# Kernel optimization log

Hardware: AMD Instinct MI355X
Metric: run time of the kernel (lower is better)

Reference implementation:

```python
import jax, jax.numpy as jnp
import numpy as np


def setup_inputs() -> dict:
    key = jax.random.key(0)
    ks = jax.random.split(key, 20)
    B, N, C = 8, 16384, 3

    def w(k, shape, scale=0.1):
        return jax.random.normal(k, shape, dtype=jnp.float32) * scale

    inp = {
        "points": jax.random.normal(ks[0], (B, N, C), dtype=jnp.float32),
        # first_layer: Conv1d(3,64,k=1)+BN+ReLU  (BN folded to scale s, shift t)
        "w0": w(ks[1], (64, 3)), "b0": w(ks[2], (64,)),
        "s0": 1.0 + w(ks[3], (64,), 0.05), "t0": w(ks[4], (64,), 0.05),
        # mlp1[3:]: Conv1d(64,64,k=1)+BN+ReLU
        "w1": w(ks[5], (64, 64)), "b1": w(ks[6], (64,)),
        "s1": 1.0 + w(ks[7], (64,), 0.05), "t1": w(ks[8], (64,), 0.05),
        # mlp2: Conv1d(64,128)+BN+ReLU, Conv1d(128,1024)+BN+ReLU
        "w2": w(ks[9], (128, 64)), "b2": w(ks[10], (128,)),
        "s2": 1.0 + w(ks[11], (128,), 0.05), "t2": w(ks[12], (128,), 0.05),
        "w3": w(ks[13], (1024, 128)), "b3": w(ks[14], (1024,)),
        "s3": 1.0 + w(ks[15], (1024,), 0.05), "t3": w(ks[16], (1024,), 0.05),
        "M": 512,
        "R": 32,
    }
    return inp


def _block(h, w, b, s, t):
    # pointwise Conv1d (k=1) + eval-mode BatchNorm (folded affine) + ReLU
    y = jnp.einsum('bmri,oi->bmro', h, w) + b
    return jax.nn.relu(y * s + t)


def reference(points, w0, b0, s0, t0, w1, b1, s1, t1,
              w2, b2, s2, t2, w3, b3, s3, t3, M, R):
    B, N, C = points.shape
    xyz = points[..., :3]
    barange = jnp.arange(B)

    # --- sampling: iteratively pick point farthest from the LAST centroid
    # (faithful to the original, which uses only centroids[i], not min-dist FPS)
    def step(last, _):
        d = jnp.sqrt(jnp.sum((xyz - last[:, None, :3]) ** 2, axis=-1))  # [B,N]
        ind = jnp.argmax(d, axis=-1)                                    # [B]
        new = points[barange, ind]                                      # [B,C]
        return new, new

    first = points[:, 0]  # deterministic stand-in for the random initial index
    _, rest = jax.lax.scan(step, first, None, length=M - 1)
    centroids = jnp.concatenate(
        [first[:, None], jnp.swapaxes(rest, 0, 1)], axis=1)  # [B,M,C]

    # --- grouping: R nearest points to each centroid
    d = jnp.sqrt(jnp.sum(
        (xyz[:, None] - centroids[:, :, None, :3]) ** 2, axis=-1))  # [B,M,N]
    _, idx = jax.lax.top_k(-d, R)                                    # [B,M,R]
    groups = points[barange[:, None, None], idx]                     # [B,M,R,C]

    # --- pointnet: shared pointwise MLP + max over group, vectorized over M
    h = _block(groups, w0, b0, s0, t0)   # [B,M,R,64]
    h = _block(h, w1, b1, s1, t1)        # [B,M,R,64]
    h = _block(h, w2, b2, s2, t2)        # [B,M,R,128]
    h = _block(h, w3, b3, s3, t3)        # [B,M,R,1024]
    g = jnp.max(h, axis=2)               # [B,M,1024]
    return g[..., None]                  # [B,M,1024,1]
```

## Files before the change

### kernel.cpp

```cpp
#include <hip/hip_runtime.h>

#define NPT 16384
#define MC  512
#define BATCH 8
#define CAP 512
#define LCAP 128

typedef __attribute__((ext_vector_type(8))) __bf16 bf16x8;
typedef __attribute__((ext_vector_type(4))) float f32x4;
typedef __attribute__((ext_vector_type(16))) float f32x16;
typedef __attribute__((ext_vector_type(2))) float f32x2;

static __device__ __forceinline__ unsigned short f2bf(float f) {
    unsigned int u = __float_as_uint(f);
    unsigned int r = (u + 0x7FFFu + ((u >> 16) & 1u)) >> 16;
    return (unsigned short)r;
}

static __device__ __forceinline__ float dist2(float x, float y, float z,
                                              float cx, float cy, float cz) {
    float dx = x - cx, dy = y - cy, dz = z - cz;
    return __fadd_rn(__fadd_rn(__fmul_rn(dx, dx), __fmul_rn(dy, dy)), __fmul_rn(dz, dz));
}

static __device__ __forceinline__ void dist2_pair(f32x2 x, f32x2 y, f32x2 z,
                                                  float cx, float cy, float cz,
                                                  float& d0, float& d1) {
    float dx0 = x[0] - cx, dx1 = x[1] - cx;
    float dy0 = y[0] - cy, dy1 = y[1] - cy;
    float dz0 = z[0] - cz, dz1 = z[1] - cz;
    float a0 = __fmul_rn(dx0, dx0), a1 = __fmul_rn(dx1, dx1);
    float b0 = __fmul_rn(dy0, dy0), b1 = __fmul_rn(dy1, dy1);
    float c0 = __fmul_rn(dz0, dz0), c1 = __fmul_rn(dz1, dz1);
    d0 = __fadd_rn(__fadd_rn(a0, b0), c0);
    d1 = __fadd_rn(__fadd_rn(a1, b1), c1);
}

__global__ void prep_all(const float* __restrict__ points,
                         const float* __restrict__ w1, const float* __restrict__ b1,
                         const float* __restrict__ s1, const float* __restrict__ t1,
                         const float* __restrict__ w2, const float* __restrict__ b2,
                         const float* __restrict__ s2, const float* __restrict__ t2,
                         const float* __restrict__ w3, const float* __restrict__ b3,
                         const float* __restrict__ s3, const float* __restrict__ t3,
                         unsigned short* __restrict__ Wp1, unsigned short* __restrict__ Wp2,
                         unsigned short* __restrict__ Wp3,
                         float* __restrict__ bias1, float* __restrict__ bias2,
                         float* __restrict__ bias3, float* __restrict__ soa,
                         int* __restrict__ gcnt) {
    int i = blockIdx.x * blockDim.x + threadIdx.x;
    if (i < 64 * 64) {
        int o = i >> 6;
        Wp1[i] = f2bf(w1[i] * s1[o]);
    } else if (i < 64 * 64 + 128 * 64) {
        int j = i - 4096; int o = j >> 6;
        Wp2[j] = f2bf(w2[j] * s2[o]);
    } else if (i < 64 * 64 + 128 * 64 + 1024 * 128) {
        int j = i - 12288; int o = j >> 7; int col = j & 127;
        int scol = (((col >> 3) ^ (o & 7)) << 3) | (col & 7);
        Wp3[j] = f2bf(w3[(o << 7) | scol] * s3[o]);
    }
    if (i < 64)   bias1[i] = b1[i] * s1[i] + t1[i];
    if (i < 128)  bias2[i] = b2[i] * s2[i] + t2[i];
    if (i < 1024) bias3[i] = b3[i] * s3[i] + t3[i];
    if (i < BATCH * MC) gcnt[i] = 0;
    if (i < BATCH * NPT) {
        int b = i >> 14, j = i & (NPT - 1);
        const float* p = points + ((size_t)b * NPT + j) * 3;
        float* s = soa + (size_t)b * 3 * NPT;
        s[j] = p[0];
        s[NPT + j] = p[1];
        s[2 * NPT + j] = p[2];
    }
}

__global__ __launch_bounds__(1024) void fps_kernel(const float* __restrict__ pts,
                                                   float* __restrict__ cent) {
    int b = blockIdx.x;
    const float* P = pts + (size_t)b * NPT * 3;
    float* C = cent + (size_t)b * MC * 3;
    __shared__ int hist[MC];
    __shared__ float curx, cury, curz;
    __shared__ float rd[16];
    __shared__ int ri[16];
    __shared__ int s_found, s_j;

    int tid = threadIdx.x;
    int i0 = tid * 16;
    float px[16], py[16], pz[16];
#pragma unroll
    for (int j = 0; j < 16; j++) {
        px[j] = P[(i0 + j) * 3 + 0];
        py[j] = P[(i0 + j) * 3 + 1];
        pz[j] = P[(i0 + j) * 3 + 2];
    }
    if (tid == 0) {
        hist[0] = 0;
        curx = P[0]; cury = P[1]; curz = P[2];
        C[0] = P[0]; C[1] = P[1]; C[2] = P[2];
        s_found = 0; s_j = 0;
    }
    __syncthreads();

    int t;
    for (t = 1; t < MC; t++) {
        float cx = curx, cy = cury, cz = curz;
        float bd = -1.0f; int bi = 0;
#pragma unroll
        for (int j = 0; j < 16; j++) {
            float dx = px[j] - cx, dy = py[j] - cy, dz = pz[j] - cz;
            float d2 = __fadd_rn(__fadd_rn(__fmul_rn(dx, dx), __fmul_rn(dy, dy)), __fmul_rn(dz, dz));
            float d = __fsqrt_rn(d2);
            if (d > bd) { bd = d; bi = i0 + j; }
        }
#pragma unroll
        for (int off = 32; off; off >>= 1) {
            float od = __shfl_xor(bd, off);
            int   oi = __shfl_xor(bi, off);
            if (od > bd || (od == bd && oi < bi)) { bd = od; bi = oi; }
        }
        int wid = tid >> 6;
        if ((tid & 63) == 0) { rd[wid] = bd; ri[wid] = bi; }
        __syncthreads();
        if (tid == 0) {
            float fb = rd[0]; int fi = ri[0];
            for (int wv = 1; wv < 16; wv++)
                if (rd[wv] > fb || (rd[wv] == fb && ri[wv] < fi)) { fb = rd[wv]; fi = ri[wv]; }
            int found = -1;
            for (int j = 0; j < t; j++) if (hist[j] == fi) { found = j; break; }
            hist[t] = fi;
            s_j = found;
            curx = P[fi * 3]; cury = P[fi * 3 + 1]; curz = P[fi * 3 + 2];
            C[t * 3] = curx; C[t * 3 + 1] = cury; C[t * 3 + 2] = curz;
            s_found = (found >= 0);
        }
        __syncthreads();
        if (s_found) break;
    }
    if (s_found && t < MC - 1) {
        int j = s_j, p = t - s_j;
        for (int k = t + 1 + tid; k < MC; k += 1024) {
            int src = j + (k - j) % p;
            int ind = hist[src];
            C[k * 3] = P[ind * 3]; C[k * 3 + 1] = P[ind * 3 + 1]; C[k * 3 + 2] = P[ind * 3 + 2];
        }
    }
}

__global__ __launch_bounds__(256) void bound_gather_kernel(
    const float* __restrict__ soa, const float* __restrict__ cent,
    int* __restrict__ gcnt, unsigned long long* __restrict__ gcand) {
    int tid = threadIdx.x, wv = tid >> 6, lane = tid & 63;
    int blk = blockIdx.x;
    int grp = blk >> 2;
    int chunk = blk & 3;
    int b = grp >> 6;
    int gbase = grp * 8;
    const float* Px = soa + (size_t)b * 3 * NPT + chunk * 4096;
    const float* Py = Px + NPT;
    const float* Pz = Py + NPT;

    __shared__ float smin[8][256];
    __shared__ unsigned int sU[8];
    __shared__ int lcnt[8];
    __shared__ unsigned long long lcand[8][LCAP];
    __shared__ int gslot[8];

    if (tid < 8) lcnt[tid] = 0;

    float cx[8], cy[8], cz[8];
#pragma unroll
    for (int c = 0; c < 8; c++) {
        cx[c] = __uint_as_float(__builtin_amdgcn_readfirstlane(__float_as_uint(cent[(size_t)(gbase + c) * 3 + 0])));
        cy[c] = __uint_as_float(__builtin_amdgcn_readfirstlane(__float_as_uint(cent[(size_t)(gbase + c) * 3 + 1])));
        cz[c] = __uint_as_float(__builtin_amdgcn_readfirstlane(__float_as_uint(cent[(size_t)(gbase + c) * 3 + 2])));
    }

    float lmin[8];
#pragma unroll
    for (int c = 0; c < 8; c++) lmin[c] = 3.4e38f;
#pragma unroll 2
    for (int k = 0; k < 8; k++) {
        int i = tid * 2 + k * 512;
        f32x2 x = *(const f32x2*)&Px[i];
        f32x2 y = *(const f32x2*)&Py[i];
        f32x2 z = *(const f32x2*)&Pz[i];
#pragma unroll
        for (int c = 0; c < 8; c++) {
            float d0, d1;
            dist2_pair(x, y, z, cx[c], cy[c], cz[c], d0, d1);
            lmin[c] = fminf(lmin[c], fminf(d0, d1));
        }
    }
#pragma unroll
    for (int c = 0; c < 8; c++) smin[c][tid] = lmin[c];
    __syncthreads();

    for (int cc = 0; cc < 2; ++cc) {
        int c = wv * 2 + cc;
        float4 q = *(const float4*)&smin[c][lane << 2];
        float m = fminf(fminf(q.x, q.y), fminf(q.z, q.w));
        unsigned int mb = __float_as_uint(m);
        unsigned int T = 0;
#pragma unroll
        for (int bit = 30; bit >= 0; --bit) {
            unsigned int cnd = T | (1u << bit);
            int cnt = __popcll(__ballot(mb < cnd));
            if (cnt <= 31) T = cnd;
        }
        float s = __fsqrt_rn(__uint_as_float(T));
        unsigned int u = T;
        for (int it = 0; it < 8 && __fsqrt_rn(__uint_as_float(u + 1u)) <= s; ++it) u++;
        if (lane == 0) sU[c] = u;
    }
    __syncthreads();
    unsigned int U[8];
#pragma unroll
    for (int c = 0; c < 8; c++) U[c] = sU[c];

#pragma unroll 2
    for (int k = 0; k < 8; k++) {
        int i = tid * 2 + k * 512;
        f32x2 x = *(const f32x2*)&Px[i];
        f32x2 y = *(const f32x2*)&Py[i];
        f32x2 z = *(const f32x2*)&Pz[i];
        unsigned int gi = (unsigned int)(chunk * 4096 + i);
#pragma unroll
        for (int c = 0; c < 8; c++) {
            float d0, d1;
            dist2_pair(x, y, z, cx[c], cy[c], cz[c], d0, d1);
            if (__float_as_uint(d0) <= U[c]) {
                int p = atomicAdd(&lcnt[c], 1);
                if (p < LCAP) {
                    unsigned int sb = __float_as_uint(__fsqrt_rn(d0));
                    lcand[c][p] = ((unsigned long long)sb << 32) | gi;
                }
            }
            if (__float_as_uint(d1) <= U[c]) {
                int p = atomicAdd(&lcnt[c], 1);
                if (p < LCAP) {
                    unsigned int sb = __float_as_uint(__fsqrt_rn(d1));
                    lcand[c][p] = ((unsigned long long)sb << 32) | (gi + 1u);
                }
            }
        }
    }
    __syncthreads();

    if (tid < 8) {
        int c = tid, n = lcnt[c];
        int add = (n > LCAP) ? 1000000 : n;
        gslot[c] = atomicAdd(&gcnt[gbase + c], add);
    }
    __syncthreads();
    for (int cc = 0; cc < 2; ++cc) {
        int c = wv * 2 + cc;
        int n = lcnt[c] < LCAP ? lcnt[c] : LCAP;
        int base = gslot[c];
        for (int q = lane; q < n; q += 64) {
            int pos = base + q;
            if (pos < CAP) gcand[(size_t)(gbase + c) * CAP + pos] = lcand[c][q];
        }
    }
}

__global__ __launch_bounds__(256) void select_l0_kernel(
    const float* __restrict__ soa, const float* __restrict__ cent,
    const int* __restrict__ gcnt, const unsigned long long* __restrict__ gcand,
    const float* __restrict__ w0, const float* __restrict__ b0,
    const float* __restrict__ s0, const float* __restrict__ t0,
    unsigned short* __restrict__ h0) {
    int tid = threadIdx.x, wv = tid >> 6, lane = tid & 63;
    int g = blockIdx.x * 4 + wv;
    int b = g >> 9;
    const float* Px = soa + (size_t)b * 3 * NPT;
    const float* Py = Px + NPT;
    const float* Pz = Py + NPT;

    __shared__ unsigned long long scand[4][CAP];
    __shared__ float sxyz[4][32][3];

    int n = gcnt[g];
    int nc = n < CAP ? n : CAP;
    for (int q = lane; q < nc; q += 64) scand[wv][q] = gcand[(size_t)g * CAP + q];

    unsigned long long sel = 0, last = 0;
    if (n <= CAP) {
        for (int s = 0; s < 32; s++) {
            unsigned long long best = ~0ull;
            for (int q = lane; q < nc; q += 64) {
                unsigned long long kk = scand[wv][q];
                if ((s == 0 || kk > last) && kk < best) best = kk;
            }
#pragma unroll
            for (int off = 32; off; off >>= 1) {
                unsigned long long o = __shfl_xor(best, off);
                best = o < best ? o : best;
            }
            last = best;
            if (lane == s) sel = best;
        }
    } else {
        for (int s = 0; s < 32; s++) {
            unsigned long long best = ~0ull;
            float ccx = cent[(size_t)g * 3], ccy = cent[(size_t)g * 3 + 1], ccz = cent[(size_t)g * 3 + 2];
            for (int i = lane; i < NPT; i += 64) {
                float d2 = dist2(Px[i], Py[i], Pz[i], ccx, ccy, ccz);
                unsigned int db = __float_as_uint(__fsqrt_rn(d2));
                unsigned long long kk = ((unsigned long long)db << 32) | (unsigned int)i;
                if ((s == 0 || kk > last) && kk < best) best = kk;
            }
#pragma unroll
            for (int off = 32; off; off >>= 1) {
                unsigned long long o = __shfl_xor(best, off);
                best = o < best ? o : best;
            }
            last = best;
            if (lane == s) sel = best;
        }
    }
    if (lane < 32) {
        unsigned int idx = (unsigned int)sel;
        if (idx >= NPT) idx = 0;
        sxyz[wv][lane][0] = Px[idx];
        sxyz[wv][lane][1] = Py[idx];
        sxyz[wv][lane][2] = Pz[idx];
    }

    int o = lane;
    float sw = s0[o];
    float fw0 = w0[o * 3] * sw, fw1 = w0[o * 3 + 1] * sw, fw2 = w0[o * 3 + 2] * sw;
    float fb = b0[o] * sw + t0[o];
    size_t base = ((size_t)g * 32) * 64 + o;
#pragma unroll 8
    for (int r = 0; r < 32; r++) {
        float x = sxyz[wv][r][0], y = sxyz[wv][r][1], z = sxyz[wv][r][2];
        float acc = fmaf(z, fw2, fmaf(y, fw1, fmaf(x, fw0, fb)));
        h0[base + (size_t)r * 64] = f2bf(fmaxf(acc, 0.0f));
    }
}

template <int N>
__global__ __launch_bounds__(256) void gemm_relu_kernel(
    const unsigned short* __restrict__ A, const unsigned short* __restrict__ W,
    const float* __restrict__ bias, unsigned short* __restrict__ Out) {
    __shared__ unsigned short sW[N * 64];
    int tid = threadIdx.x, w = tid >> 6, lane = tid & 63, lr = lane & 15, lq = lane >> 4;
    const int SWEEPS = (N * 64 * 2) / 4096;
#pragma unroll
    for (int sweep = 0; sweep < SWEEPS; ++sweep) {
        int r = sweep * 32 + (tid >> 3), s = tid & 7;
        int ss = s ^ (r & 7);
        *(uint4*)&sW[r * 64 + s * 8] = *(const uint4*)&W[r * 64 + ss * 8];
    }
    __syncthreads();

    int row0 = blockIdx.x * 256 + w * 64;
    const int NT = N / 16;
    f32x4 acc[4][NT];
#pragma unroll
    for (int m = 0; m < 4; m++)
#pragma unroll
        for (int n = 0; n < NT; n++) acc[m][n] = (f32x4){0.f, 0.f, 0.f, 0.f};

    bf16x8 a[4][2];
#pragma unroll
    for (int m = 0; m < 4; m++)
#pragma unroll
        for (int ks = 0; ks < 2; ks++)
            a[m][ks] = *(const bf16x8*)&A[(size_t)(row0 + m * 16 + lr) * 64 + ks * 32 + lq * 8];

#pragma unroll
    for (int ks = 0; ks < 2; ks++)
#pragma unroll
        for (int n = 0; n < NT; n++) {
            bf16x8 wf = *(const bf16x8*)&sW[(n * 16 + lr) * 64 + (((ks * 4 + lq) ^ (lr & 7)) * 8)];
#pragma unroll
            for (int m = 0; m < 4; m++)
                acc[m][n] = __builtin_amdgcn_mfma_f32_16x16x32_bf16(a[m][ks], wf, acc[m][n], 0, 0, 0);
        }

#pragma unroll
    for (int n = 0; n < NT; n++) {
        int col = n * 16 + lr;
        float bb = bias[col];
#pragma unroll
        for (int m = 0; m < 4; m++)
#pragma unroll
            for (int i = 0; i < 4; i++) {
                int rr = row0 + m * 16 + lq * 4 + i;
                Out[(size_t)rr * N + col] = f2bf(fmaxf(acc[m][n][i] + bb, 0.f));
            }
    }
}

__global__ __launch_bounds__(256) void gemm3_max_kernel(
    const unsigned short* __restrict__ A, const unsigned short* __restrict__ W,
    const float* __restrict__ bias, float* __restrict__ Out) {
    __shared__ unsigned short sW[128 * 128];
    int tid = threadIdx.x, w = tid >> 6, lane = tid & 63;
    int l32 = lane & 31, hi = lane >> 5;
    int wr = w >> 1, wc = w & 1;
    int row0 = blockIdx.x * 128 + wr * 64;
    int g0 = row0 >> 5;

    bf16x8 a[2][8];
#pragma unroll
    for (int m = 0; m < 2; m++)
#pragma unroll
        for (int ks = 0; ks < 8; ks++)
            a[m][ks] = *(const bf16x8*)&A[(size_t)(row0 + m * 32 + l32) * 128 + ks * 16 + hi * 8];

    for (int cb = 0; cb < 8; ++cb) {
#pragma unroll
        for (int j = 0; j < 8; ++j) {
            const unsigned short* g = W + (size_t)cb * 16384 + w * 4096 + j * 512 + lane * 8;
            __builtin_amdgcn_global_load_lds(
                (const __attribute__((address_space(1))) void*)g,
                (__attribute__((address_space(3))) void*)&sW[w * 4096 + j * 512],
                16, 0, 0);
        }
        __syncthreads();

        f32x16 acc[2][2];
#pragma unroll
        for (int m = 0; m < 2; m++)
#pragma unroll
            for (int n = 0; n < 2; n++)
#pragma unroll
                for (int r = 0; r < 16; r++) acc[m][n][r] = 0.f;

#pragma unroll
        for (int ks = 0; ks < 8; ks++)
#pragma unroll
            for (int n = 0; n < 2; n++) {
                int rw = wc * 64 + n * 32 + l32;
                int slot = (ks * 2 + hi) ^ (rw & 7);
                bf16x8 wf = *(const bf16x8*)&sW[rw * 128 + slot * 8];
#pragma unroll
                for (int m = 0; m < 2; m++)
                    acc[m][n] = __builtin_amdgcn_mfma_f32_32x32x16_bf16(a[m][ks], wf, acc[m][n], 0, 0, 0);
            }

#pragma unroll
        for (int n = 0; n < 2; n++) {
            int col = cb * 128 + wc * 64 + n * 32 + l32;
            float bb = bias[col];
#pragma unroll
            for (int m = 0; m < 2; m++) {
                float t0_ = fmaxf(acc[m][n][0], acc[m][n][1]);
                float t1_ = fmaxf(acc[m][n][2], acc[m][n][3]);
                float t2_ = fmaxf(acc[m][n][4], acc[m][n][5]);
                float t3_ = fmaxf(acc[m][n][6], acc[m][n][7]);
                float t4_ = fmaxf(acc[m][n][8], acc[m][n][9]);
                float t5_ = fmaxf(acc[m][n][10], acc[m][n][11]);
                float t6_ = fmaxf(acc[m][n][12], acc[m][n][13]);
                float t7_ = fmaxf(acc[m][n][14], acc[m][n][15]);
                float u0 = fmaxf(t0_, t1_), u1 = fmaxf(t2_, t3_);
                float u2 = fmaxf(t4_, t5_), u3 = fmaxf(t6_, t7_);
                float v = fmaxf(fmaxf(u0, u1), fmaxf(u2, u3));
                v = fmaxf(v, __shfl_xor(v, 32));
                v = fmaxf(v + bb, 0.f);
                if (hi == 0) Out[(size_t)(g0 + m) * 1024 + col] = v;
            }
        }
        __syncthreads();
    }
}

extern "C" void kernel_launch(void* const* d_in, const int* in_sizes, int n_in,
                              void* d_out, int out_size, void* d_ws, size_t ws_size,
                              hipStream_t stream) {
    const float* points = (const float*)d_in[0];
    const float* w0 = (const float*)d_in[1];
    const float* b0 = (const float*)d_in[2];
    const float* s0 = (const float*)d_in[3];
    const float* t0 = (const float*)d_in[4];
    const float* w1 = (const float*)d_in[5];
    const float* b1 = (const float*)d_in[6];
    const float* s1 = (const float*)d_in[7];
    const float* t1 = (const float*)d_in[8];
    const float* w2 = (const float*)d_in[9];
    const float* b2 = (const float*)d_in[10];
    const float* s2 = (const float*)d_in[11];
    const float* t2 = (const float*)d_in[12];
    const float* w3 = (const float*)d_in[13];
    const float* b3 = (const float*)d_in[14];
    const float* s3 = (const float*)d_in[15];
    const float* t3 = (const float*)d_in[16];

    char* ws = (char*)d_ws;
    float* cent = (float*)(ws + 0);
    unsigned short* Wp1 = (unsigned short*)(ws + 49152);
    unsigned short* Wp2 = (unsigned short*)(ws + 57344);
    unsigned short* Wp3 = (unsigned short*)(ws + 73728);
    float* bias1 = (float*)(ws + 335872);
    float* bias2 = (float*)(ws + 336128);
    float* bias3 = (float*)(ws + 336640);
    unsigned short* h0 = (unsigned short*)(ws + 340736);
    unsigned short* h1 = (unsigned short*)(ws + 340736 + 16777216);
    unsigned short* h2 = (unsigned short*)(ws + 340736 + 2 * 16777216);
    int* gcnt = (int*)(ws + 340736 + 3 * 16777216);
    float* soa = (float*)h2;
    unsigned long long* gcand = (unsigned long long*)h1;
    float* out = (float*)d_out;

    hipLaunchKernelGGL(prep_all, dim3(560), dim3(256), 0, stream,
                       points, w1, b1, s1, t1, w2, b2, s2, t2, w3, b3, s3, t3,
                       Wp1, Wp2, Wp3, bias1, bias2, bias3, soa, gcnt);
    hipLaunchKernelGGL(fps_kernel, dim3(BATCH), dim3(1024), 0, stream, points, cent);
    hipLaunchKernelGGL(bound_gather_kernel, dim3(2048), dim3(256), 0, stream,
                       soa, cent, gcnt, gcand);
    hipLaunchKernelGGL(select_l0_kernel, dim3(1024), dim3(256), 0, stream,
                       soa, cent, gcnt, gcand, w0, b0, s0, t0, h0);
    hipLaunchKernelGGL((gemm_relu_kernel<64>), dim3(512), dim3(256), 0, stream, h0, Wp1, bias1, h1);
    hipLaunchKernelGGL((gemm_relu_kernel<128>), dim3(512), dim3(256), 0, stream, h1, Wp2, bias2, h2);
    hipLaunchKernelGGL(gemm3_max_kernel, dim3(1024), dim3(256), 0, stream, h2, Wp3, bias3, out);
}
```

Baseline: 169.6 us.

## Use float4 AoS points with precomputed norms and expanded distance bound

Replaces the SoA x/y/z point copy with a float4 layout that stores each point's squared norm. The bound pass now computes squared distance as |p|^2+|c|^2-2p·c with FMAs, using one vector load per point instead of three. The candidate filter adds an epsilon margin to allow for rounding error, and exact distances are computed only for accepted candidates. This cuts ALU and load work in the bounding kernel, but the epsilon may admit more candidates and risks overflowing LCAP. Storing the norm also raises the bytes read per point.

```diff
diff --git a/kernel.cpp b/kernel.cpp
--- a/kernel.cpp
+++ b/kernel.cpp
@@ -9,7 +9,6 @@
 typedef __attribute__((ext_vector_type(8))) __bf16 bf16x8;
 typedef __attribute__((ext_vector_type(4))) float f32x4;
 typedef __attribute__((ext_vector_type(16))) float f32x16;
-typedef __attribute__((ext_vector_type(2))) float f32x2;
 
 static __device__ __forceinline__ unsigned short f2bf(float f) {
     unsigned int u = __float_as_uint(f);
@@ -21,19 +20,6 @@
                                               float cx, float cy, float cz) {
     float dx = x - cx, dy = y - cy, dz = z - cz;
     return __fadd_rn(__fadd_rn(__fmul_rn(dx, dx), __fmul_rn(dy, dy)), __fmul_rn(dz, dz));
-}
-
-static __device__ __forceinline__ void dist2_pair(f32x2 x, f32x2 y, f32x2 z,
-                                                  float cx, float cy, float cz,
-                                                  float& d0, float& d1) {
-    float dx0 = x[0] - cx, dx1 = x[1] - cx;
-    float dy0 = y[0] - cy, dy1 = y[1] - cy;
-    float dz0 = z[0] - cz, dz1 = z[1] - cz;
-    float a0 = __fmul_rn(dx0, dx0), a1 = __fmul_rn(dx1, dx1);
-    float b0 = __fmul_rn(dy0, dy0), b1 = __fmul_rn(dy1, dy1);
-    float c0 = __fmul_rn(dz0, dz0), c1 = __fmul_rn(dz1, dz1);
-    d0 = __fadd_rn(__fadd_rn(a0, b0), c0);
-    d1 = __fadd_rn(__fadd_rn(a1, b1), c1);
 }
 
 __global__ void prep_all(const float* __restrict__ points,
@@ -46,7 +32,7 @@
                          unsigned short* __restrict__ Wp1, unsigned short* __restrict__ Wp2,
                          unsigned short* __restrict__ Wp3,
                          float* __restrict__ bias1, float* __restrict__ bias2,
-                         float* __restrict__ bias3, float* __restrict__ soa,
+                         float* __restrict__ bias3, float4* __restrict__ pts4,
                          int* __restrict__ gcnt) {
     int i = blockIdx.x * blockDim.x + threadIdx.x;
     if (i < 64 * 64) {
@@ -65,12 +51,9 @@
     if (i < 1024) bias3[i] = b3[i] * s3[i] + t3[i];
     if (i < BATCH * MC) gcnt[i] = 0;
     if (i < BATCH * NPT) {
-        int b = i >> 14, j = i & (NPT - 1);
-        const float* p = points + ((size_t)b * NPT + j) * 3;
-        float* s = soa + (size_t)b * 3 * NPT;
-        s[j] = p[0];
-        s[NPT + j] = p[1];
-        s[2 * NPT + j] = p[2];
+        const float* p = points + (size_t)i * 3;
+        float x = p[0], y = p[1], z = p[2];
+        pts4[i] = make_float4(x, y, z, x * x + y * y + z * z);
     }
 }
 
@@ -148,7 +131,7 @@
 }
 
 __global__ __launch_bounds__(256) void bound_gather_kernel(
-    const float* __restrict__ soa, const float* __restrict__ cent,
+    const float4* __restrict__ pts4, const float* __restrict__ cent,
     int* __restrict__ gcnt, unsigned long long* __restrict__ gcand) {
     int tid = threadIdx.x, wv = tid >> 6, lane = tid & 63;
     int blk = blockIdx.x;
@@ -156,40 +139,36 @@
     int chunk = blk & 3;
     int b = grp >> 6;
     int gbase = grp * 8;
-    const float* Px = soa + (size_t)b * 3 * NPT + chunk * 4096;
-    const float* Py = Px + NPT;
-    const float* Pz = Py + NPT;
+    const float4* P4 = pts4 + (size_t)b * NPT + chunk * 4096;
 
     __shared__ float smin[8][256];
-    __shared__ unsigned int sU[8];
+    __shared__ float sB[8];
     __shared__ int lcnt[8];
     __shared__ unsigned long long lcand[8][LCAP];
     __shared__ int gslot[8];
 
     if (tid < 8) lcnt[tid] = 0;
 
-    float cx[8], cy[8], cz[8];
+    float cx[8], cy[8], cz[8], hc[8];
 #pragma unroll
     for (int c = 0; c < 8; c++) {
         cx[c] = __uint_as_float(__builtin_amdgcn_readfirstlane(__float_as_uint(cent[(size_t)(gbase + c) * 3 + 0])));
         cy[c] = __uint_as_float(__builtin_amdgcn_readfirstlane(__float_as_uint(cent[(size_t)(gbase + c) * 3 + 1])));
         cz[c] = __uint_as_float(__builtin_amdgcn_readfirstlane(__float_as_uint(cent[(size_t)(gbase + c) * 3 + 2])));
+        hc[c] = cx[c] * cx[c] + cy[c] * cy[c] + cz[c] * cz[c];
     }
 
     float lmin[8];
 #pragma unroll
     for (int c = 0; c < 8; c++) lmin[c] = 3.4e38f;
-#pragma unroll 2
-    for (int k = 0; k < 8; k++) {
-        int i = tid * 2 + k * 512;
-        f32x2 x = *(const f32x2*)&Px[i];
-        f32x2 y = *(const f32x2*)&Py[i];
-        f32x2 z = *(const f32x2*)&Pz[i];
+#pragma unroll 4
+    for (int k = 0; k < 16; k++) {
+        float4 p = P4[tid + k * 256];
 #pragma unroll
         for (int c = 0; c < 8; c++) {
-            float d0, d1;
-            dist2_pair(x, y, z, cx[c], cy[c], cz[c], d0, d1);
-            lmin[c] = fminf(lmin[c], fminf(d0, d1));
+            float t = fmaf(p.x, cx[c], fmaf(p.y, cy[c], p.z * cz[c]));
+            float d2 = fmaxf(fmaf(-2.0f, t, p.w + hc[c]), 0.0f);
+            lmin[c] = fminf(lmin[c], d2);
         }
     }
 #pragma unroll
@@ -208,39 +187,30 @@
             int cnt = __popcll(__ballot(mb < cnd));
             if (cnt <= 31) T = cnd;
         }
-        float s = __fsqrt_rn(__uint_as_float(T));
-        unsigned int u = T;
-        for (int it = 0; it < 8 && __fsqrt_rn(__uint_as_float(u + 1u)) <= s; ++it) u++;
-        if (lane == 0) sU[c] = u;
-    }
-    __syncthreads();
-    unsigned int U[8];
-#pragma unroll
-    for (int c = 0; c < 8; c++) U[c] = sU[c];
-
-#pragma unroll 2
-    for (int k = 0; k < 8; k++) {
-        int i = tid * 2 + k * 512;
-        f32x2 x = *(const f32x2*)&Px[i];
-        f32x2 y = *(const f32x2*)&Py[i];
-        f32x2 z = *(const f32x2*)&Pz[i];
-        unsigned int gi = (unsigned int)(chunk * 4096 + i);
+        if (lane == 0) sB[c] = __uint_as_float(T);
+    }
+    __syncthreads();
+    float Bf[8];
+#pragma unroll
+    for (int c = 0; c < 8; c++) Bf[c] = sB[c];
+
+#pragma unroll 4
+    for (int k = 0; k < 16; k++) {
+        int il = tid + k * 256;
+        float4 p = P4[il];
+        unsigned int gi = (unsigned int)(chunk * 4096 + il);
 #pragma unroll
         for (int c = 0; c < 8; c++) {
-            float d0, d1;
-            dist2_pair(x, y, z, cx[c], cy[c], cz[c], d0, d1);
-            if (__float_as_uint(d0) <= U[c]) {
-                int p = atomicAdd(&lcnt[c], 1);
-                if (p < LCAP) {
-                    unsigned int sb = __float_as_uint(__fsqrt_rn(d0));
-                    lcand[c][p] = ((unsigned long long)sb << 32) | gi;
-                }
-            }
-            if (__float_as_uint(d1) <= U[c]) {
-                int p = atomicAdd(&lcnt[c], 1);
-                if (p < LCAP) {
-                    unsigned int sb = __float_as_uint(__fsqrt_rn(d1));
-                    lcand[c][p] = ((unsigned long long)sb << 32) | (gi + 1u);
+            float s = p.w + hc[c];
+            float t = fmaf(p.x, cx[c], fmaf(p.y, cy[c], p.z * cz[c]));
+            float d2f = fmaf(-2.0f, t, s);
+            float eps = fmaf(8e-7f, s, 4e-6f);
+            if (d2f - eps <= Bf[c]) {
+                int pslot = atomicAdd(&lcnt[c], 1);
+                if (pslot < LCAP) {
+                    float d2x = dist2(p.x, p.y, p.z, cx[c], cy[c], cz[c]);
+                    unsigned int sb = __float_as_uint(__fsqrt_rn(d2x));
+                    lcand[c][pslot] = ((unsigned long long)sb << 32) | gi;
                 }
             }
         }
@@ -265,7 +235,7 @@
 }
 
 __global__ __launch_bounds__(256) void select_l0_kernel(
-    const float* __restrict__ soa, const float* __restrict__ cent,
+    const float4* __restrict__ pts4, const float* __restrict__ cent,
     const int* __restrict__ gcnt, const unsigned long long* __restrict__ gcand,
     const float* __restrict__ w0, const float* __restrict__ b0,
     const float* __restrict__ s0, const float* __restrict__ t0,
@@ -273,9 +243,7 @@
     int tid = threadIdx.x, wv = tid >> 6, lane = tid & 63;
     int g = blockIdx.x * 4 + wv;
     int b = g >> 9;
-    const float* Px = soa + (size_t)b * 3 * NPT;
-    const float* Py = Px + NPT;
-    const float* Pz = Py + NPT;
+    const float4* P4 = pts4 + (size_t)b * NPT;
 
     __shared__ unsigned long long scand[4][CAP];
     __shared__ float sxyz[4][32][3];
@@ -305,7 +273,8 @@
             unsigned long long best = ~0ull;
             float ccx = cent[(size_t)g * 3], ccy = cent[(size_t)g * 3 + 1], ccz = cent[(size_t)g * 3 + 2];
             for (int i = lane; i < NPT; i += 64) {
-                float d2 = dist2(Px[i], Py[i], Pz[i], ccx, ccy, ccz);
+                float4 p = P4[i];
+                float d2 = dist2(p.x, p.y, p.z, ccx, ccy, ccz);
                 unsigned int db = __float_as_uint(__fsqrt_rn(d2));
                 unsigned long long kk = ((unsigned long long)db << 32) | (unsigned int)i;
                 if ((s == 0 || kk > last) && kk < best) best = kk;
@@ -322,9 +291,10 @@
     if (lane < 32) {
         unsigned int idx = (unsigned int)sel;
         if (idx >= NPT) idx = 0;
-        sxyz[wv][lane][0] = Px[idx];
-        sxyz[wv][lane][1] = Py[idx];
-        sxyz[wv][lane][2] = Pz[idx];
+        float4 p = P4[idx];
+        sxyz[wv][lane][0] = p.x;
+        sxyz[wv][lane][1] = p.y;
+        sxyz[wv][lane][2] = p.z;
     }
 
     int o = lane;
@@ -501,18 +471,18 @@
     unsigned short* h1 = (unsigned short*)(ws + 340736 + 16777216);
     unsigned short* h2 = (unsigned short*)(ws + 340736 + 2 * 16777216);
     int* gcnt = (int*)(ws + 340736 + 3 * 16777216);
-    float* soa = (float*)h2;
+    float4* pts4 = (float4*)h2;
     unsigned long long* gcand = (unsigned long long*)h1;
     float* out = (float*)d_out;
 
     hipLaunchKernelGGL(prep_all, dim3(560), dim3(256), 0, stream,
                        points, w1, b1, s1, t1, w2, b2, s2, t2, w3, b3, s3, t3,
-                       Wp1, Wp2, Wp3, bias1, bias2, bias3, soa, gcnt);
+                       Wp1, Wp2, Wp3, bias1, bias2, bias3, pts4, gcnt);
     hipLaunchKernelGGL(fps_kernel, dim3(BATCH), dim3(1024), 0, stream, points, cent);
     hipLaunchKernelGGL(bound_gather_kernel, dim3(2048), dim3(256), 0, stream,
-                       soa, cent, gcnt, gcand);
+                       pts4, cent, gcnt, gcand);
     hipLaunchKernelGGL(select_l0_kernel, dim3(1024), dim3(256), 0, stream,
-                       soa, cent, gcnt, gcand, w0, b0, s0, t0, h0);
+                       pts4, cent, gcnt, gcand, w0, b0, s0, t0, h0);
     hipLaunchKernelGGL((gemm_relu_kernel<64>), dim3(512), dim3(256), 0, stream, h0, Wp1, bias1, h1);
     hipLaunchKernelGGL((gemm_relu_kernel<128>), dim3(512), dim3(256), 0, stream, h1, Wp2, bias2, h2);
     hipLaunchKernelGGL(gemm3_max_kernel, dim3(1024), dim3(256), 0, stream, h2, Wp3, bias3, out);
```

New measurement: 174.0 us. 1.03x slower.
